# Optimization experiments

Hardware: AMD Instinct MI355X
Metric: run time of the kernel (lower is better)

Reference implementation:

```python
import jax, jax.numpy as jnp
import numpy as np

H = 8  # num_heads (init kwarg)

def setup_inputs() -> dict:
    key = jax.random.key(0)
    k1, k2, k3, k4 = jax.random.split(key, 4)
    B, S, E = 4, 2048, 512
    x = jax.random.normal(k1, (B, S, E), dtype=jnp.float32)
    # 'normal' keras initializer ~ N(0, 0.05)
    Wq = jax.random.normal(k2, (E, E), dtype=jnp.float32) * 0.05
    Wk = jax.random.normal(k3, (E, E), dtype=jnp.float32) * 0.05
    Wv = jax.random.normal(k4, (E, E), dtype=jnp.float32) * 0.05
    return {"x": x, "Wq": Wq, "Wk": Wk, "Wv": Wv}

def _split_heads(t):
    # [B,S,E] -> [H,B,S,E/H]; matches tf.stack(tf.split(t, H, axis=2))
    B, S, E = t.shape
    return t.reshape(B, S, H, E // H).transpose(2, 0, 1, 3)

def reference(x, Wq, Wk, Wv):
    B, S, E = x.shape
    q = _split_heads(jnp.einsum('bse,ef->bsf', x, Wq))  # [H,B,S,dh]
    k = _split_heads(jnp.einsum('bse,ef->bsf', x, Wk))
    v = _split_heads(jnp.einsum('bse,ef->bsf', x, Wv))
    # NOTE: original has NO 1/sqrt(d) scaling
    scores = jnp.einsum('hbqd,hbkd->hbqk', q, k)         # [H,B,S,S]
    attn = jax.nn.softmax(scores, axis=-1)
    effect = jnp.einsum('hbqk,hbkd->hbqd', attn, v)      # [H,B,S,dh]
    # tf.concat(tf.split(effect, H), axis=-1) + squeeze == merge heads on last dim
    out = effect.transpose(1, 2, 0, 3).reshape(B, S, E)  # [B,S,E]
    return (out, x)
```

## Files before the change

### kernel.cpp

```cpp
#include <hip/hip_runtime.h>

typedef _Float16 f16x8 __attribute__((ext_vector_type(8)));
typedef __fp16 h16x2 __attribute__((ext_vector_type(2)));
typedef float f32x4 __attribute__((ext_vector_type(4)));
typedef float f32x16 __attribute__((ext_vector_type(16)));

#define GF(r) ((((r)&3)) ^ (((r)>>2)&3))
#define LOG2E 1.44269504088896f

#define GLD16(gp, lp) __builtin_amdgcn_global_load_lds( \
    (const __attribute__((address_space(1))) void*)(gp), \
    (__attribute__((address_space(3))) void*)(lp), 16, 0, 0)

__global__ void cvt_x_kernel(const float4* __restrict__ x4, f16x8* __restrict__ xh,
                             float4* __restrict__ xc, int n8) {
    int i = blockIdx.x * 256 + threadIdx.x;
    if (i >= n8) return;
    float4 a = x4[2 * i], b = x4[2 * i + 1];
    xc[2 * i] = a;
    xc[2 * i + 1] = b;
    f16x8 h;
    h[0] = (_Float16)a.x; h[1] = (_Float16)a.y; h[2] = (_Float16)a.z; h[3] = (_Float16)a.w;
    h[4] = (_Float16)b.x; h[5] = (_Float16)b.y; h[6] = (_Float16)b.z; h[7] = (_Float16)b.w;
    xh[i] = h;
}

__global__ void cvt_w_kernel(const float* __restrict__ Wq, const float* __restrict__ Wk,
                             const float* __restrict__ Wv, _Float16* __restrict__ wt) {
    int j = blockIdx.x * 256 + threadIdx.x;
    if (j >= 786432) return;
    int mat = j >> 18;
    int r = (j >> 9) & 511;
    int n = j & 511;
    const float* W = (mat == 0) ? Wq : ((mat == 1) ? Wk : Wv);
    float v = W[r * 512 + n];
    wt[(size_t)mat * 262144 + (size_t)n * 512 + r] = (_Float16)v;
}

__global__ __launch_bounds__(256, 2) void gemm_qkv(
    const _Float16* __restrict__ xh, const _Float16* __restrict__ wt,
    _Float16* __restrict__ qh, _Float16* __restrict__ kh, _Float16* __restrict__ vt) {
    __shared__ __align__(16) char gsm[49152];
    const int mat = blockIdx.y;
    const _Float16* wp = wt + (size_t)mat * 262144;
    const int mtile = blockIdx.x >> 2, ntile = blockIdx.x & 3;
    const int tid = threadIdx.x, lane = tid & 63;
    const int g = lane >> 4, c = lane & 15;
    const int wid = tid >> 6, wm = wid >> 1, wn = wid & 1;

    f32x4 acc[4][4];
#pragma unroll
    for (int i = 0; i < 4; ++i)
#pragma unroll
        for (int j = 0; j < 4; ++j) acc[i][j] = (f32x4){0.f, 0.f, 0.f, 0.f};

    const int row0 = tid >> 2, p0 = tid & 3;

    auto GSTAGE = [&](int buf, int ks) {
        _Float16* la_ = (_Float16*)(gsm + buf * 16384);
        _Float16* lb_ = (_Float16*)(gsm + buf * 16384 + 8192);
        int r = row0, pp = p0 ^ GF(r);
        GLD16(xh + (size_t)(mtile * 128 + r) * 512 + ks * 32 + pp * 8, &la_[tid * 8]);
        GLD16(wp + (size_t)(ntile * 128 + r) * 512 + ks * 32 + pp * 8, &lb_[tid * 8]);
        r = 64 + row0; pp = p0 ^ GF(r);
        GLD16(xh + (size_t)(mtile * 128 + r) * 512 + ks * 32 + pp * 8, &la_[(256 + tid) * 8]);
        GLD16(wp + (size_t)(ntile * 128 + r) * 512 + ks * 32 + pp * 8, &lb_[(256 + tid) * 8]);
    };

    auto GTILE = [&](int ks) {
        const _Float16* la = (const _Float16*)(gsm + (ks % 3) * 16384);
        const _Float16* lb = (const _Float16*)(gsm + (ks % 3) * 16384 + 8192);
        f16x8 af[4], bf[4];
#pragma unroll
        for (int i = 0; i < 4; ++i) {
            int ra = wm * 64 + i * 16 + c;
            af[i] = *(const f16x8*)&la[ra * 32 + ((g ^ GF(ra)) * 8)];
            int rb = wn * 64 + i * 16 + c;
            bf[i] = *(const f16x8*)&lb[rb * 32 + ((g ^ GF(rb)) * 8)];
        }
        __builtin_amdgcn_s_setprio(1);
#pragma unroll
        for (int mi = 0; mi < 4; ++mi)
#pragma unroll
            for (int ni = 0; ni < 4; ++ni)
                acc[mi][ni] = __builtin_amdgcn_mfma_f32_16x16x32_f16(af[mi], bf[ni], acc[mi][ni], 0, 0, 0);
        __builtin_amdgcn_s_setprio(0);
    };

    GSTAGE(0, 0); GSTAGE(1, 1);
#pragma unroll 1
    for (int ks = 0; ks < 14; ++ks) {
        asm volatile("s_waitcnt vmcnt(4)" ::: "memory");
        __builtin_amdgcn_s_barrier();
        __builtin_amdgcn_sched_barrier(0);
        GSTAGE((ks + 2) % 3, ks + 2);
        GTILE(ks);
    }
    asm volatile("s_waitcnt vmcnt(4)" ::: "memory");
    __builtin_amdgcn_s_barrier();
    GTILE(14);
    asm volatile("s_waitcnt vmcnt(0)" ::: "memory");
    __builtin_amdgcn_s_barrier();
    GTILE(15);

#pragma unroll
    for (int mi = 0; mi < 4; ++mi)
#pragma unroll
        for (int ni = 0; ni < 4; ++ni)
#pragma unroll
            for (int r = 0; r < 4; ++r) {
                int m = mtile * 128 + wm * 64 + mi * 16 + g * 4 + r;
                int n = ntile * 128 + wn * 64 + ni * 16 + c;
                _Float16 hv = (_Float16)acc[mi][ni][r];
                if (mat == 0) {
                    qh[(size_t)m * 512 + n] = hv;
                } else if (mat == 1) {
                    kh[(size_t)m * 512 + n] = hv;
                } else {
                    int h = n >> 6, d = n & 63, bb = m >> 11, s = m & 2047;
                    vt[(((size_t)h * 4 + bb) * 64 + d) * 2048 + s] = hv;
                }
            }
}

__global__ __launch_bounds__(256, 2) void attn_kernel(
    const _Float16* __restrict__ qh, const _Float16* __restrict__ kh,
    const _Float16* __restrict__ vt, float* __restrict__ out) {
    __shared__ __align__(16) char smem[65536];

    const int bid = blockIdx.x;
    const int xcd = bid & 7, idx = bid >> 3;
    const int hb = xcd * 4 + (idx >> 4);
    const int qblk = idx & 15;
    const int h = hb >> 2, b = hb & 3;
    const int tid = threadIdx.x, lane = tid & 63, wid = tid >> 6;
    const int q = lane & 31, hi = lane >> 5;

    const int qrow0 = qblk * 128 + wid * 32;
    const _Float16* qp = qh + ((size_t)b * 2048 + qrow0) * 512 + h * 64;
    const _Float16* kp = kh + (size_t)b * 2048 * 512 + h * 64;
    const _Float16* vp = vt + (size_t)hb * 64 * 2048;

    const int srow = tid >> 3;
    const int ssw = (tid & 7) ^ (srow & 7);

    auto STAGE = [&](int buf, int kt) {
        _Float16* kb_ = (_Float16*)(smem + buf * 16384);
        _Float16* vb_ = (_Float16*)(smem + buf * 16384 + 8192);
        GLD16(kp + ((size_t)(kt * 64 + srow) * 512) + ssw * 8, &kb_[tid * 8]);
        GLD16(kp + ((size_t)(kt * 64 + srow + 32) * 512) + ssw * 8, &kb_[(tid + 256) * 8]);
        GLD16(vp + (size_t)srow * 2048 + kt * 64 + ssw * 8, &vb_[tid * 8]);
        GLD16(vp + (size_t)(srow + 32) * 2048 + kt * 64 + ssw * 8, &vb_[(tid + 256) * 8]);
    };

    f16x8 aQ[4];
#pragma unroll
    for (int kc = 0; kc < 4; ++kc)
        aQ[kc] = *(const f16x8*)(qp + (size_t)q * 512 + kc * 16 + hi * 8);

    float mrow = -1e30f, lrow = 0.f;
    f32x16 o0, o1;
#pragma unroll
    for (int i = 0; i < 16; ++i) { o0[i] = 0.f; o1[i] = 0.f; }

    const h16x2 ONE2 = {(__fp16)1.0f, (__fp16)1.0f};

    auto TILE = [&](int kt) {
        const _Float16* kb = (const _Float16*)(smem + (kt & 3) * 16384);
        const _Float16* vb = (const _Float16*)(smem + (kt & 3) * 16384 + 8192);

        f32x16 s0, s1;
        __builtin_amdgcn_s_setprio(1);
        {
            f32x16 z0, z1;
#pragma unroll
            for (int i = 0; i < 16; ++i) { z0[i] = 0.f; z1[i] = 0.f; }
            const int r0 = q, r1 = 32 + q, sw = q & 7;
#pragma unroll
            for (int kc = 0; kc < 4; ++kc) {
                f16x8 ak0 = *(const f16x8*)&kb[r0 * 64 + (((2 * kc + hi) ^ sw) * 8)];
                f16x8 ak1 = *(const f16x8*)&kb[r1 * 64 + (((2 * kc + hi) ^ sw) * 8)];
                z0 = __builtin_amdgcn_mfma_f32_32x32x16_f16(ak0, aQ[kc], z0, 0, 0, 0);
                z1 = __builtin_amdgcn_mfma_f32_32x32x16_f16(ak1, aQ[kc], z1, 0, 0, 0);
            }
            s0 = z0; s1 = z1;
        }
        __builtin_amdgcn_s_setprio(0);

        float pm;
        {
            float m0 = fmaxf(fmaxf(fmaxf(s0[0], s0[1]), s0[2]), s0[3]);
            float m1 = fmaxf(fmaxf(fmaxf(s0[4], s0[5]), s0[6]), s0[7]);
            float m2 = fmaxf(fmaxf(fmaxf(s0[8], s0[9]), s0[10]), s0[11]);
            float m3 = fmaxf(fmaxf(fmaxf(s0[12], s0[13]), s0[14]), s0[15]);
            float m4 = fmaxf(fmaxf(fmaxf(s1[0], s1[1]), s1[2]), s1[3]);
            float m5 = fmaxf(fmaxf(fmaxf(s1[4], s1[5]), s1[6]), s1[7]);
            float m6 = fmaxf(fmaxf(fmaxf(s1[8], s1[9]), s1[10]), s1[11]);
            float m7 = fmaxf(fmaxf(fmaxf(s1[12], s1[13]), s1[14]), s1[15]);
            float t0 = fmaxf(fmaxf(m0, m1), m2);
            float t1 = fmaxf(fmaxf(m3, m4), m5);
            float t2 = fmaxf(m6, m7);
            pm = fmaxf(fmaxf(t0, t1), t2);
        }
        pm = fmaxf(pm, __shfl_xor(pm, 32));
        if (__any(pm > mrow + 8.0f)) {
            const float nm = fmaxf(mrow, pm);
            const float e = __builtin_amdgcn_exp2f((mrow - nm) * LOG2E);
            mrow = nm;
            lrow *= e;
            o0 *= e;
            o1 *= e;
        }
        const float nm2 = mrow * LOG2E;

#pragma unroll
        for (int i = 0; i < 16; ++i)
            s0[i] = __builtin_amdgcn_exp2f(fmaf(s0[i], LOG2E, -nm2));
#pragma unroll
        for (int i = 0; i < 16; ++i)
            s1[i] = __builtin_amdgcn_exp2f(fmaf(s1[i], LOG2E, -nm2));

        f16x8 pf[4];
        float rs = 0.f;
#pragma unroll
        for (int kb2 = 0; kb2 < 2; ++kb2) {
            const f32x16& sv = kb2 ? s1 : s0;
            h16x2 p0 = __builtin_amdgcn_cvt_pkrtz(sv[0], sv[1]);
            h16x2 p1 = __builtin_amdgcn_cvt_pkrtz(sv[2], sv[3]);
            h16x2 p2 = __builtin_amdgcn_cvt_pkrtz(sv[4], sv[5]);
            h16x2 p3 = __builtin_amdgcn_cvt_pkrtz(sv[6], sv[7]);
            h16x2 p4 = __builtin_amdgcn_cvt_pkrtz(sv[8], sv[9]);
            h16x2 p5 = __builtin_amdgcn_cvt_pkrtz(sv[10], sv[11]);
            h16x2 p6 = __builtin_amdgcn_cvt_pkrtz(sv[12], sv[13]);
            h16x2 p7 = __builtin_amdgcn_cvt_pkrtz(sv[14], sv[15]);
            rs = __builtin_amdgcn_fdot2(p0, ONE2, rs, false);
            rs = __builtin_amdgcn_fdot2(p1, ONE2, rs, false);
            rs = __builtin_amdgcn_fdot2(p2, ONE2, rs, false);
            rs = __builtin_amdgcn_fdot2(p3, ONE2, rs, false);
            rs = __builtin_amdgcn_fdot2(p4, ONE2, rs, false);
            rs = __builtin_amdgcn_fdot2(p5, ONE2, rs, false);
            rs = __builtin_amdgcn_fdot2(p6, ONE2, rs, false);
            rs = __builtin_amdgcn_fdot2(p7, ONE2, rs, false);
            unsigned t0 = __builtin_bit_cast(unsigned, p0);
            unsigned t1 = __builtin_bit_cast(unsigned, p1);
            unsigned t2 = __builtin_bit_cast(unsigned, p2);
            unsigned t3 = __builtin_bit_cast(unsigned, p3);
            unsigned t4 = __builtin_bit_cast(unsigned, p4);
            unsigned t5 = __builtin_bit_cast(unsigned, p5);
            unsigned t6 = __builtin_bit_cast(unsigned, p6);
            unsigned t7 = __builtin_bit_cast(unsigned, p7);
            asm volatile("v_permlane32_swap_b32 %0, %1" : "+v"(t0), "+v"(t2));
            asm volatile("v_permlane32_swap_b32 %0, %1" : "+v"(t1), "+v"(t3));
            asm volatile("v_permlane32_swap_b32 %0, %1" : "+v"(t4), "+v"(t6));
            asm volatile("v_permlane32_swap_b32 %0, %1" : "+v"(t5), "+v"(t7));
            uint4 u0; u0.x = t0; u0.y = t1; u0.z = t2; u0.w = t3;
            uint4 u1; u1.x = t4; u1.y = t5; u1.z = t6; u1.w = t7;
            pf[2 * kb2 + 0] = __builtin_bit_cast(f16x8, u0);
            pf[2 * kb2 + 1] = __builtin_bit_cast(f16x8, u1);
        }
        lrow += rs;

        __builtin_amdgcn_s_setprio(1);
        {
            const int d0 = q, d1 = 32 + q, sw = q & 7;
#pragma unroll
            for (int ck = 0; ck < 4; ++ck) {
                f16x8 av0 = *(const f16x8*)&vb[d0 * 64 + (((2 * ck + hi) ^ sw) * 8)];
                f16x8 av1 = *(const f16x8*)&vb[d1 * 64 + (((2 * ck + hi) ^ sw) * 8)];
                o0 = __builtin_amdgcn_mfma_f32_32x32x16_f16(av0, pf[ck], o0, 0, 0, 0);
                o1 = __builtin_amdgcn_mfma_f32_32x32x16_f16(av1, pf[ck], o1, 0, 0, 0);
            }
        }
        __builtin_amdgcn_s_setprio(0);
    };

    STAGE(0, 0); STAGE(1, 1); STAGE(2, 2);
#pragma unroll 1
    for (int kt = 0; kt < 29; ++kt) {
        asm volatile("s_waitcnt vmcnt(8)" ::: "memory");
        __builtin_amdgcn_s_barrier();
        __builtin_amdgcn_sched_barrier(0);
        STAGE((kt + 3) & 3, kt + 3);
        TILE(kt);
    }
    asm volatile("s_waitcnt vmcnt(8)" ::: "memory");
    __builtin_amdgcn_s_barrier();
    TILE(29);
    asm volatile("s_waitcnt vmcnt(4)" ::: "memory");
    __builtin_amdgcn_s_barrier();
    TILE(30);
    asm volatile("s_waitcnt vmcnt(0)" ::: "memory");
    __builtin_amdgcn_s_barrier();
    TILE(31);

    __syncthreads();
    lrow += __shfl_xor(lrow, 32);
    const float inv = 1.0f / lrow;
    float* ebw = (float*)smem + wid * 2112;
#pragma unroll
    for (int i = 0; i < 16; ++i) {
        int dr = (i & 3) + 8 * (i >> 2) + 4 * hi;
        ebw[dr * 33 + q] = o0[i] * inv;
        ebw[(32 + dr) * 33 + q] = o1[i] * inv;
    }
    __builtin_amdgcn_s_waitcnt(0);
    const int d0c = (lane & 15) * 4;
#pragma unroll
    for (int i = 0; i < 8; ++i) {
        int qr = 4 * i + (lane >> 4);
        float4 v;
        v.x = ebw[(d0c + 0) * 33 + qr];
        v.y = ebw[(d0c + 1) * 33 + qr];
        v.z = ebw[(d0c + 2) * 33 + qr];
        v.w = ebw[(d0c + 3) * 33 + qr];
        *(float4*)(out + ((size_t)b * 2048 + qrow0 + qr) * 512 + h * 64 + d0c) = v;
    }
}

extern "C" void kernel_launch(void* const* d_in, const int* in_sizes, int n_in,
                              void* d_out, int out_size, void* d_ws, size_t ws_size,
                              hipStream_t stream) {
    const float* x = (const float*)d_in[0];
    const float* Wq = (const float*)d_in[1];
    const float* Wk = (const float*)d_in[2];
    const float* Wv = (const float*)d_in[3];
    float* out = (float*)d_out;
    float* xcopy = out + 4194304;

    char* ws = (char*)d_ws;
    _Float16* xh = (_Float16*)ws;
    _Float16* wt = (_Float16*)(ws + (size_t)(10u << 20));
    _Float16* qh = (_Float16*)(ws + (size_t)(12u << 20));
    _Float16* kh = (_Float16*)(ws + (size_t)(20u << 20));
    _Float16* vt = (_Float16*)(ws + (size_t)(28u << 20));

    cvt_x_kernel<<<2048, 256, 0, stream>>>((const float4*)x, (f16x8*)xh, (float4*)xcopy, 524288);
    cvt_w_kernel<<<3072, 256, 0, stream>>>(Wq, Wk, Wv, wt);
    gemm_qkv<<<dim3(256, 3), 256, 0, stream>>>(xh, wt, qh, kh, vt);
    attn_kernel<<<512, 256, 0, stream>>>(qh, kh, vt, out);
}
```

Before: 95.51 us.

## Split attention KV range across two wave groups and merge partial softmax

The attention block grows to 512 threads. Two halves of the waves each process half of the key/value sequence for the same 128 query rows, and their partial softmax state (max, sum, output) is merged through shared memory at the end. Staging changes from a 4-deep single-tile ring to a double buffer that loads both halves' tiles each iteration, with a full vmcnt(0) wait. This doubles waves per query block to hide latency, at the cost of a shallower prefetch, an extra merge pass through LDS, and launch bounds that may force fewer registers per thread.

```diff
diff --git a/kernel.cpp b/kernel.cpp
--- a/kernel.cpp
+++ b/kernel.cpp
@@ -123,7 +123,7 @@
             }
 }
 
-__global__ __launch_bounds__(256, 2) void attn_kernel(
+__global__ __launch_bounds__(512, 4) void attn_kernel(
     const _Float16* __restrict__ qh, const _Float16* __restrict__ kh,
     const _Float16* __restrict__ vt, float* __restrict__ out) {
     __shared__ __align__(16) char smem[65536];
@@ -134,9 +134,10 @@
     const int qblk = idx & 15;
     const int h = hb >> 2, b = hb & 3;
     const int tid = threadIdx.x, lane = tid & 63, wid = tid >> 6;
+    const int qg = wid & 3, half = wid >> 2;
     const int q = lane & 31, hi = lane >> 5;
 
-    const int qrow0 = qblk * 128 + wid * 32;
+    const int qrow0 = qblk * 128 + qg * 32;
     const _Float16* qp = qh + ((size_t)b * 2048 + qrow0) * 512 + h * 64;
     const _Float16* kp = kh + (size_t)b * 2048 * 512 + h * 64;
     const _Float16* vp = vt + (size_t)hb * 64 * 2048;
@@ -144,13 +145,12 @@
     const int srow = tid >> 3;
     const int ssw = (tid & 7) ^ (srow & 7);
 
-    auto STAGE = [&](int buf, int kt) {
-        _Float16* kb_ = (_Float16*)(smem + buf * 16384);
-        _Float16* vb_ = (_Float16*)(smem + buf * 16384 + 8192);
-        GLD16(kp + ((size_t)(kt * 64 + srow) * 512) + ssw * 8, &kb_[tid * 8]);
-        GLD16(kp + ((size_t)(kt * 64 + srow + 32) * 512) + ssw * 8, &kb_[(tid + 256) * 8]);
-        GLD16(vp + (size_t)srow * 2048 + kt * 64 + ssw * 8, &vb_[tid * 8]);
-        GLD16(vp + (size_t)(srow + 32) * 2048 + kt * 64 + ssw * 8, &vb_[(tid + 256) * 8]);
+    auto STAGE = [&](int i) {
+        char* base = smem + (i & 1) * 32768;
+        GLD16(kp + ((size_t)(i * 64 + srow) * 512) + ssw * 8, (_Float16*)(base) + tid * 8);
+        GLD16(vp + (size_t)srow * 2048 + i * 64 + ssw * 8, (_Float16*)(base + 8192) + tid * 8);
+        GLD16(kp + ((size_t)((16 + i) * 64 + srow) * 512) + ssw * 8, (_Float16*)(base + 16384) + tid * 8);
+        GLD16(vp + (size_t)srow * 2048 + (16 + i) * 64 + ssw * 8, (_Float16*)(base + 24576) + tid * 8);
     };
 
     f16x8 aQ[4];
@@ -165,9 +165,9 @@
 
     const h16x2 ONE2 = {(__fp16)1.0f, (__fp16)1.0f};
 
-    auto TILE = [&](int kt) {
-        const _Float16* kb = (const _Float16*)(smem + (kt & 3) * 16384);
-        const _Float16* vb = (const _Float16*)(smem + (kt & 3) * 16384 + 8192);
+    auto TILE = [&](int it) {
+        const _Float16* kb = (const _Float16*)(smem + (it & 1) * 32768 + half * 16384);
+        const _Float16* vb = kb + 4096;
 
         f32x16 s0, s1;
         __builtin_amdgcn_s_setprio(1);
@@ -274,46 +274,60 @@
         __builtin_amdgcn_s_setprio(0);
     };
 
-    STAGE(0, 0); STAGE(1, 1); STAGE(2, 2);
+    STAGE(0);
 #pragma unroll 1
-    for (int kt = 0; kt < 29; ++kt) {
-        asm volatile("s_waitcnt vmcnt(8)" ::: "memory");
+    for (int it = 0; it < 16; ++it) {
+        asm volatile("s_waitcnt vmcnt(0)" ::: "memory");
         __builtin_amdgcn_s_barrier();
         __builtin_amdgcn_sched_barrier(0);
-        STAGE((kt + 3) & 3, kt + 3);
-        TILE(kt);
+        if (it < 15) STAGE(it + 1);
+        TILE(it);
     }
-    asm volatile("s_waitcnt vmcnt(8)" ::: "memory");
+
+    lrow += __shfl_xor(lrow, 32);
     __builtin_amdgcn_s_barrier();
-    TILE(29);
-    asm volatile("s_waitcnt vmcnt(4)" ::: "memory");
-    __builtin_amdgcn_s_barrier();
-    TILE(30);
-    asm volatile("s_waitcnt vmcnt(0)" ::: "memory");
-    __builtin_amdgcn_s_barrier();
-    TILE(31);
-
+
+    float* xg = (float*)smem + qg * 2112;
+    if (half) {
+#pragma unroll
+        for (int i = 0; i < 16; ++i) {
+            xg[i * 64 + lane] = o0[i];
+            xg[(16 + i) * 64 + lane] = o1[i];
+        }
+        if (!hi) { xg[2048 + q] = mrow; xg[2080 + q] = lrow; }
+    }
     __syncthreads();
-    lrow += __shfl_xor(lrow, 32);
-    const float inv = 1.0f / lrow;
-    float* ebw = (float*)smem + wid * 2112;
-#pragma unroll
-    for (int i = 0; i < 16; ++i) {
-        int dr = (i & 3) + 8 * (i >> 2) + 4 * hi;
-        ebw[dr * 33 + q] = o0[i] * inv;
-        ebw[(32 + dr) * 33 + q] = o1[i] * inv;
-    }
-    __builtin_amdgcn_s_waitcnt(0);
-    const int d0c = (lane & 15) * 4;
-#pragma unroll
-    for (int i = 0; i < 8; ++i) {
-        int qr = 4 * i + (lane >> 4);
-        float4 v;
-        v.x = ebw[(d0c + 0) * 33 + qr];
-        v.y = ebw[(d0c + 1) * 33 + qr];
-        v.z = ebw[(d0c + 2) * 33 + qr];
-        v.w = ebw[(d0c + 3) * 33 + qr];
-        *(float4*)(out + ((size_t)b * 2048 + qrow0 + qr) * 512 + h * 64 + d0c) = v;
+    if (!half) {
+        const float m_b = xg[2048 + q], l_b = xg[2080 + q];
+        const float m = fmaxf(mrow, m_b);
+        const float e_a = __builtin_amdgcn_exp2f((mrow - m) * LOG2E);
+        const float e_b = __builtin_amdgcn_exp2f((m_b - m) * LOG2E);
+        const float inv = 1.0f / (lrow * e_a + l_b * e_b);
+        const float sa = e_a * inv, sb = e_b * inv;
+#pragma unroll
+        for (int i = 0; i < 16; ++i) {
+            o0[i] = o0[i] * sa + xg[i * 64 + lane] * sb;
+            o1[i] = o1[i] * sa + xg[(16 + i) * 64 + lane] * sb;
+        }
+        asm volatile("s_waitcnt lgkmcnt(0)" ::: "memory");
+#pragma unroll
+        for (int i = 0; i < 16; ++i) {
+            int dr = (i & 3) + 8 * (i >> 2) + 4 * hi;
+            xg[dr * 33 + q] = o0[i];
+            xg[(32 + dr) * 33 + q] = o1[i];
+        }
+        __builtin_amdgcn_s_waitcnt(0);
+        const int d0c = (lane & 15) * 4;
+#pragma unroll
+        for (int i2 = 0; i2 < 8; ++i2) {
+            int qr = 4 * i2 + (lane >> 4);
+            float4 v;
+            v.x = xg[(d0c + 0) * 33 + qr];
+            v.y = xg[(d0c + 1) * 33 + qr];
+            v.z = xg[(d0c + 2) * 33 + qr];
+            v.w = xg[(d0c + 3) * 33 + qr];
+            *(float4*)(out + ((size_t)b * 2048 + qrow0 + qr) * 512 + h * 64 + d0c) = v;
+        }
     }
 }
 
@@ -337,5 +351,5 @@
     cvt_x_kernel<<<2048, 256, 0, stream>>>((const float4*)x, (f16x8*)xh, (float4*)xcopy, 524288);
     cvt_w_kernel<<<3072, 256, 0, stream>>>(Wq, Wk, Wv, wt);
     gemm_qkv<<<dim3(256, 3), 256, 0, stream>>>(xh, wt, qh, kh, vt);
-    attn_kernel<<<512, 256, 0, stream>>>(qh, kh, vt, out);
-}
+    attn_kernel<<<512, 512, 0, stream>>>(qh, kh, vt, out);
+}
```

New measurement: 93.54 us. 2.1% less time.
